# Kernel tuning notes

Measured on AMD Instinct MI355X. Metric: run time of the kernel, lower is better.

The kernel has to match this reference:

```python
import jax, jax.numpy as jnp
import numpy as np

SEQ_LEN = 2048
VOCAB = 32000
N_EMBD = 768
D_INNER = 1536
D_STATE = 16
D_CONV = 4
DT_RANK = 48
N_LAYERS = 2
EPS = 1e-5


def setup_inputs() -> dict:
    key = jax.random.key(0)
    ks = jax.random.split(key, 10)
    s = 0.02
    tokens = jax.random.randint(ks[0], (SEQ_LEN,), 0, VOCAB)
    E = jax.random.normal(ks[1], (VOCAB, N_EMBD)) * s  # tied embedding / lm_head
    in_proj_w = jax.random.normal(ks[2], (N_LAYERS, 2 * D_INNER, N_EMBD)) * s
    conv_w = jax.random.normal(ks[3], (N_LAYERS, D_INNER, 1, D_CONV)) * s  # depthwise
    conv_b = jax.random.normal(ks[4], (N_LAYERS, D_INNER)) * s
    x_proj_w = jax.random.normal(ks[5], (N_LAYERS, DT_RANK + 2 * D_STATE, D_INNER)) * s
    dt_proj_w = jax.random.normal(ks[6], (N_LAYERS, D_INNER, DT_RANK)) * s
    dt_proj_b = jax.random.normal(ks[7], (N_LAYERS, D_INNER)) * s
    # A init exactly as in the module: repeat(arange(1,d_state+1), d_inner).reshape(d_inner, d_state)
    A = jnp.repeat(jnp.arange(1, D_STATE + 1), D_INNER).reshape(D_INNER, D_STATE).astype(jnp.float32)
    A_log = jnp.broadcast_to(jnp.log(A), (N_LAYERS, D_INNER, D_STATE))
    D_param = jnp.ones((N_LAYERS, D_INNER))
    out_proj_w = jax.random.normal(ks[8], (N_LAYERS, N_EMBD, D_INNER)) * s
    norm_w = jnp.ones((N_LAYERS, N_EMBD))
    norm_b = jnp.zeros((N_LAYERS, N_EMBD))
    normf_w = jnp.ones((N_EMBD,))
    normf_b = jnp.zeros((N_EMBD,))
    return {
        'tokens': tokens, 'E': E, 'in_proj_w': in_proj_w, 'conv_w': conv_w,
        'conv_b': conv_b, 'x_proj_w': x_proj_w, 'dt_proj_w': dt_proj_w,
        'dt_proj_b': dt_proj_b, 'A_log': A_log, 'D_param': D_param,
        'out_proj_w': out_proj_w, 'norm_w': norm_w, 'norm_b': norm_b,
        'normf_w': normf_w, 'normf_b': normf_b,
    }


def _rmsnorm(x, w, b):
    inv = jax.lax.rsqrt(jnp.mean(x * x, axis=-1, keepdims=True) + EPS)
    return x * inv * w + b


def _selective_scan(u, delta, A, B, C, D):
    # u,delta: [L, d_inner]; A: [d_inner, d_state]; B,C: [L, d_state]; D: [d_inner]
    dA = jnp.exp(jnp.einsum('ld,dn->ldn', delta, A))            # [L, d_inner, d_state]
    dBu = (delta * u)[:, :, None] * B[:, None, :]               # [L, d_inner, d_state]

    def step(x, inp):
        dA_t, dBu_t, C_t = inp
        x = dA_t * x + dBu_t
        y = x @ C_t                                             # [d_inner]
        return x, y

    x0 = jnp.zeros((D_INNER, D_STATE), dtype=u.dtype)
    _, ys = jax.lax.scan(step, x0, (dA, dBu, C))
    return ys + u * D


def _mamba_block(xn, in_w, cw, cb, xp_w, dt_w, dt_b, a_log, d_p, out_w):
    L = xn.shape[0]
    x_and_res = xn @ in_w.T                                     # [L, 2*d_inner]
    x, res = jnp.split(x_and_res, 2, axis=-1)
    # depthwise causal conv with padding d_conv-1 (both sides), then crop to L
    xc = jax.lax.conv_general_dilated(
        x.T[None], cw, window_strides=(1,), padding=[(D_CONV - 1, D_CONV - 1)],
        feature_group_count=D_INNER, dimension_numbers=('NCH', 'OIH', 'NCH'))[0]
    x = (xc[:, :L] + cb[:, None]).T                             # [L, d_inner]
    x = jax.nn.silu(x)
    # ssm
    A = -jnp.exp(a_log)
    x_dbl = x @ xp_w.T                                          # [L, dt_rank + 2*d_state]
    delta, B, C = jnp.split(x_dbl, [DT_RANK, DT_RANK + D_STATE], axis=-1)
    delta = jax.nn.softplus(delta @ dt_w.T + dt_b)              # [L, d_inner]
    y = _selective_scan(x, delta, A, B, C, d_p)
    y = y * jax.nn.silu(res)
    return y @ out_w.T                                          # [L, n_embd]


def reference(tokens, E, in_proj_w, conv_w, conv_b, x_proj_w, dt_proj_w,
              dt_proj_b, A_log, D_param, out_proj_w, norm_w, norm_b,
              normf_w, normf_b):
    h = E[tokens]                                               # [L, n_embd]
    for i in range(N_LAYERS):
        h = h + _mamba_block(_rmsnorm(h, norm_w[i], norm_b[i]),
                             in_proj_w[i], conv_w[i], conv_b[i], x_proj_w[i],
                             dt_proj_w[i], dt_proj_b[i], A_log[i], D_param[i],
                             out_proj_w[i])
    h = _rmsnorm(h, normf_w, normf_b)
    logits = h @ E.T                                            # tied lm head
    return logits
```

## Files before the change

kernel.cpp:

```cpp
#include <hip/hip_runtime.h>
#include <hip/hip_bf16.h>

#define SEQ   2048
#define NE    768
#define DI    1536
#define DS    16
#define DC    4
#define DTR   48
#define NL    2
#define VOCAB 32000
#define EPS   1e-5f
#define CHUNK 128
#define NCH   (SEQ / CHUNK)

typedef __hip_bfloat16 bf16;
typedef __bf16 bf16x8 __attribute__((ext_vector_type(8)));
typedef float  f32x4  __attribute__((ext_vector_type(4)));

#define GLOBAL_AS __attribute__((address_space(1)))
#define LDS_AS    __attribute__((address_space(3)))

__device__ __forceinline__ void gload16(const void* g, void* l)
{
    __builtin_amdgcn_global_load_lds((const GLOBAL_AS void*)g, (LDS_AS void*)l, 16, 0, 0);
}

__global__ __launch_bounds__(256) void f2b_k(const float* __restrict__ x,
    bf16* __restrict__ y, int n)
{
    int i = (blockIdx.x * 256 + threadIdx.x) * 4;
    if (i >= n) return;
    float4 v = *reinterpret_cast<const float4*>(x + i);
    y[i + 0] = __float2bfloat16(v.x);
    y[i + 1] = __float2bfloat16(v.y);
    y[i + 2] = __float2bfloat16(v.z);
    y[i + 3] = __float2bfloat16(v.w);
}

__global__ __launch_bounds__(256) void embed_k(const int* __restrict__ tok,
    const float* __restrict__ E, float* __restrict__ h)
{
    int l = blockIdx.x;
    int t = tok[l];
    for (int k = threadIdx.x; k < NE; k += 256)
        h[(size_t)l * NE + k] = E[(size_t)t * NE + k];
}

__global__ __launch_bounds__(256) void rmsnorm_k(const float* __restrict__ x,
    const float* __restrict__ w, const float* __restrict__ b, bf16* __restrict__ out)
{
    int l = blockIdx.x;
    const float* xr = x + (size_t)l * NE;
    float ss = 0.f;
    for (int k = threadIdx.x; k < NE; k += 256) { float v = xr[k]; ss += v * v; }
    for (int o = 32; o; o >>= 1) ss += __shfl_down(ss, o);
    __shared__ float s4[4];
    if ((threadIdx.x & 63) == 0) s4[threadIdx.x >> 6] = ss;
    __syncthreads();
    float inv = rsqrtf((s4[0] + s4[1] + s4[2] + s4[3]) / NE + EPS);
    for (int k = threadIdx.x; k < NE; k += 256)
        out[(size_t)l * NE + k] = __float2bfloat16(xr[k] * inv * w[k] + b[k]);
}

__global__ __launch_bounds__(256) void gemm_bt(const bf16* __restrict__ Abf,
    const bf16* __restrict__ Bbf, float* __restrict__ Cout, int M, int N, int K)
{
    __shared__ __align__(16) __bf16 As[128 * 32];
    __shared__ __align__(16) __bf16 Bs[128 * 32];

    const int tid  = threadIdx.x;
    const int wave = tid >> 6;
    const int lane = tid & 63;
    const int wm = wave >> 1, wn = wave & 1;
    const int tm = blockIdx.y * 128;
    const int tn = blockIdx.x * 128;
    const int r16 = lane & 15, quad = lane >> 4;

    const __bf16* A = reinterpret_cast<const __bf16*>(Abf);
    const __bf16* B = reinterpret_cast<const __bf16*>(Bbf);

    const int c0 = tid, c1 = tid + 256;
    const __bf16* ga0 = A + (size_t)(tm + (c0 >> 2)) * K + (c0 & 3) * 8;
    const __bf16* ga1 = A + (size_t)(tm + (c1 >> 2)) * K + (c1 & 3) * 8;
    const __bf16* gb0 = B + (size_t)(tn + (c0 >> 2)) * K + (c0 & 3) * 8;
    const __bf16* gb1 = B + (size_t)(tn + (c1 >> 2)) * K + (c1 & 3) * 8;
    __bf16* la0 = As + c0 * 8;
    __bf16* la1 = As + c1 * 8;
    __bf16* lb0 = Bs + c0 * 8;
    __bf16* lb1 = Bs + c1 * 8;

    f32x4 zero = {0.f, 0.f, 0.f, 0.f};
    f32x4 acc[4][4];
#pragma unroll
    for (int i = 0; i < 4; i++)
#pragma unroll
        for (int j = 0; j < 4; j++) acc[i][j] = zero;

    const int arow = wm * 64 + r16;
    const int brow = wn * 64 + r16;

    for (int kt = 0; kt < K; kt += 32) {
        __syncthreads();
        gload16(ga0 + kt, la0);
        gload16(ga1 + kt, la1);
        gload16(gb0 + kt, lb0);
        gload16(gb1 + kt, lb1);
        __syncthreads();

        bf16x8 av[4], bv[4];
#pragma unroll
        for (int i = 0; i < 4; i++)
            av[i] = *reinterpret_cast<const bf16x8*>(As + (arow + i * 16) * 32 + quad * 8);
#pragma unroll
        for (int j = 0; j < 4; j++)
            bv[j] = *reinterpret_cast<const bf16x8*>(Bs + (brow + j * 16) * 32 + quad * 8);
#pragma unroll
        for (int i = 0; i < 4; i++)
#pragma unroll
            for (int j = 0; j < 4; j++)
                acc[i][j] = __builtin_amdgcn_mfma_f32_16x16x32_bf16(av[i], bv[j], acc[i][j], 0, 0, 0);
    }

#pragma unroll
    for (int i = 0; i < 4; i++) {
        int cm0 = tm + wm * 64 + i * 16 + quad * 4;
#pragma unroll
        for (int j = 0; j < 4; j++) {
            int cn = tn + wn * 64 + j * 16 + r16;
#pragma unroll
            for (int r = 0; r < 4; r++)
                Cout[(size_t)(cm0 + r) * N + cn] = acc[i][j][r];
        }
    }
}

__global__ __launch_bounds__(256) void conv_silu_k(const float* __restrict__ xr,
    const float* __restrict__ cw, const float* __restrict__ cb, float* __restrict__ u)
{
    int idx = blockIdx.x * 256 + threadIdx.x;
    int l = idx / DI, d = idx - l * DI;
    float s = cb[d];
#pragma unroll
    for (int t = 0; t < DC; t++) {
        int ls = l - (DC - 1) + t;
        if (ls >= 0) s += xr[(size_t)ls * (2 * DI) + d] * cw[d * DC + t];
    }
    u[idx] = s / (1.f + expf(-s));
}

__global__ __launch_bounds__(256) void xproj_k(const float* __restrict__ u,
    const float* __restrict__ xpw, float* __restrict__ xdbl)
{
    int gw = blockIdx.x * 4 + (threadIdx.x >> 6);
    int l = gw / 80, j = gw - l * 80;
    int lane = threadIdx.x & 63;
    const float* ur = u + (size_t)l * DI;
    const float* wr = xpw + (size_t)j * DI;
    float s = 0.f;
    for (int k = lane; k < DI; k += 64) s += ur[k] * wr[k];
    for (int o = 32; o; o >>= 1) s += __shfl_down(s, o);
    if (lane == 0) xdbl[(size_t)l * 80 + j] = s;
}

__global__ __launch_bounds__(256) void dtproj_k(const float* __restrict__ xdbl,
    const float* __restrict__ dtw, const float* __restrict__ dtb, float* __restrict__ delta)
{
    int l = blockIdx.y;
    int d = blockIdx.x * 256 + threadIdx.x;
    __shared__ float xs[DTR];
    if (threadIdx.x < DTR) xs[threadIdx.x] = xdbl[(size_t)l * 80 + threadIdx.x];
    __syncthreads();
    float s = dtb[d];
    const float* wr = dtw + (size_t)d * DTR;
#pragma unroll
    for (int k = 0; k < DTR; k++) s += xs[k] * wr[k];
    delta[(size_t)l * DI + d] = fmaxf(s, 0.f) + log1pf(expf(-fabsf(s)));
}

__global__ __launch_bounds__(256) void scan1_k(const float* __restrict__ delta,
    const float* __restrict__ u, const float* __restrict__ xdbl,
    const float* __restrict__ alog, float* __restrict__ S, float* __restrict__ P)
{
    int dg = threadIdx.x >> 4, n = threadIdx.x & 15;
    int d = blockIdx.x * 16 + dg;
    int c = blockIdx.y;
    float A = -expf(alog[(size_t)d * DS + n]);
    float st = 0.f, pr = 1.f;
    int l0 = c * CHUNK;
#pragma unroll 4
    for (int t = 0; t < CHUNK; t++) {
        int l = l0 + t;
        float dl = delta[(size_t)l * DI + d];
        float ul = u[(size_t)l * DI + d];
        float Bn = xdbl[(size_t)l * 80 + DTR + n];
        float a = expf(dl * A);
        st = a * st + dl * ul * Bn;
        pr *= a;
    }
    size_t o = ((size_t)c * DI + d) * DS + n;
    S[o] = st;
    P[o] = pr;
}

__global__ __launch_bounds__(256) void scan2_k(const float* __restrict__ S,
    const float* __restrict__ P, float* __restrict__ sin_)
{
    int i = blockIdx.x * 256 + threadIdx.x;
    float run = 0.f;
#pragma unroll
    for (int c = 0; c < NCH; c++) {
        size_t o = (size_t)c * DI * DS + i;
        sin_[o] = run;
        run = S[o] + P[o] * run;
    }
}

__global__ __launch_bounds__(256) void scan3_k(const float* __restrict__ delta,
    const float* __restrict__ u, const float* __restrict__ xdbl,
    const float* __restrict__ alog, const float* __restrict__ sin_,
    const float* __restrict__ Dp, const float* __restrict__ xr,
    bf16* __restrict__ ybf)
{
    int dg = threadIdx.x >> 4, n = threadIdx.x & 15;
    int d = blockIdx.x * 16 + dg;
    int c = blockIdx.y;
    float A = -expf(alog[(size_t)d * DS + n]);
    float Dv = Dp[d];
    float st = sin_[((size_t)c * DI + d) * DS + n];
    int l0 = c * CHUNK;
#pragma unroll 2
    for (int t = 0; t < CHUNK; t++) {
        int l = l0 + t;
        float dl = delta[(size_t)l * DI + d];
        float ul = u[(size_t)l * DI + d];
        float Bn = xdbl[(size_t)l * 80 + DTR + n];
        float Cn = xdbl[(size_t)l * 80 + DTR + DS + n];
        float a = expf(dl * A);
        st = a * st + dl * ul * Bn;
        float p = st * Cn;
        p += __shfl_down(p, 8);
        p += __shfl_down(p, 4);
        p += __shfl_down(p, 2);
        p += __shfl_down(p, 1);
        if (n == 0) {
            float r = xr[(size_t)l * (2 * DI) + DI + d];
            float yv = (p + ul * Dv) * (r / (1.f + expf(-r)));
            ybf[(size_t)l * DI + d] = __float2bfloat16(yv);
        }
    }
}

__global__ __launch_bounds__(256) void add_k(float* __restrict__ h, const float* __restrict__ t)
{
    int i = blockIdx.x * 256 + threadIdx.x;
    h[i] += t[i];
}

extern "C" void kernel_launch(void* const* d_in, const int* in_sizes, int n_in,
                              void* d_out, int out_size, void* d_ws, size_t ws_size,
                              hipStream_t stream)
{
    const int*   tokens  = (const int*)  d_in[0];
    const float* E       = (const float*)d_in[1];
    const float* in_w    = (const float*)d_in[2];
    const float* conv_w  = (const float*)d_in[3];
    const float* conv_b  = (const float*)d_in[4];
    const float* xp_w    = (const float*)d_in[5];
    const float* dt_w    = (const float*)d_in[6];
    const float* dt_b    = (const float*)d_in[7];
    const float* A_log   = (const float*)d_in[8];
    const float* D_p     = (const float*)d_in[9];
    const float* out_w   = (const float*)d_in[10];
    const float* norm_w  = (const float*)d_in[11];
    const float* norm_b  = (const float*)d_in[12];
    const float* normf_w = (const float*)d_in[13];
    const float* normf_b = (const float*)d_in[14];

    char* ws = (char*)d_ws;
    size_t off = 0;
    auto alloc = [&](size_t bytes) -> void* {
        void* p = ws + off;
        off = (off + bytes + 255) & ~(size_t)255;
        return p;
    };

    float* h     = (float*)alloc((size_t)SEQ * NE * 4);
    bf16*  xn    = (bf16*) alloc((size_t)SEQ * NE * 2);
    float* xr    = (float*)alloc((size_t)SEQ * 2 * DI * 4);
    float* u     = (float*)alloc((size_t)SEQ * DI * 4);
    float* xdbl  = (float*)alloc((size_t)SEQ * 80 * 4);
    float* delta = (float*)alloc((size_t)SEQ * DI * 4);
    bf16*  ybf   = (bf16*) alloc((size_t)SEQ * DI * 2);
    float* tmp   = (float*)alloc((size_t)SEQ * NE * 4);
    bf16*  hf    = (bf16*) alloc((size_t)SEQ * NE * 2);
    bf16*  Ebf   = (bf16*) alloc((size_t)VOCAB * NE * 2);
    bf16*  wbuf  = (bf16*) alloc((size_t)2 * DI * NE * 2);
    float* Sbuf  = (float*)alloc((size_t)NCH * DI * DS * 4);
    float* Pbuf  = (float*)alloc((size_t)NCH * DI * DS * 4);
    float* Sin   = (float*)alloc((size_t)NCH * DI * DS * 4);

    {
        int n = VOCAB * NE;
        f2b_k<<<(n / 4 + 255) / 256, 256, 0, stream>>>(E, Ebf, n);
    }

    embed_k<<<SEQ, 256, 0, stream>>>(tokens, E, h);

    for (int L = 0; L < NL; L++) {
        rmsnorm_k<<<SEQ, 256, 0, stream>>>(h, norm_w + (size_t)L * NE, norm_b + (size_t)L * NE, xn);

        {
            int n = 2 * DI * NE;
            f2b_k<<<(n / 4 + 255) / 256, 256, 0, stream>>>(in_w + (size_t)L * n, wbuf, n);
        }
        gemm_bt<<<dim3(2 * DI / 128, SEQ / 128), 256, 0, stream>>>(
            xn, wbuf, xr, SEQ, 2 * DI, NE);

        conv_silu_k<<<SEQ * DI / 256, 256, 0, stream>>>(
            xr, conv_w + (size_t)L * DI * DC, conv_b + (size_t)L * DI, u);

        xproj_k<<<SEQ * 80 / 4, 256, 0, stream>>>(u, xp_w + (size_t)L * 80 * DI, xdbl);

        dtproj_k<<<dim3(DI / 256, SEQ), 256, 0, stream>>>(
            xdbl, dt_w + (size_t)L * DI * DTR, dt_b + (size_t)L * DI, delta);

        const float* alog = A_log + (size_t)L * DI * DS;
        scan1_k<<<dim3(DI / 16, NCH), 256, 0, stream>>>(delta, u, xdbl, alog, Sbuf, Pbuf);
        scan2_k<<<DI * DS / 256, 256, 0, stream>>>(Sbuf, Pbuf, Sin);
        scan3_k<<<dim3(DI / 16, NCH), 256, 0, stream>>>(
            delta, u, xdbl, alog, Sin, D_p + (size_t)L * DI, xr, ybf);

        {
            int n = NE * DI;
            f2b_k<<<(n / 4 + 255) / 256, 256, 0, stream>>>(out_w + (size_t)L * n, wbuf, n);
        }
        gemm_bt<<<dim3(NE / 128, SEQ / 128), 256, 0, stream>>>(
            ybf, wbuf, tmp, SEQ, NE, DI);

        add_k<<<SEQ * NE / 256, 256, 0, stream>>>(h, tmp);
    }

    rmsnorm_k<<<SEQ, 256, 0, stream>>>(h, normf_w, normf_b, hf);

    gemm_bt<<<dim3(VOCAB / 128, SEQ / 128), 256, 0, stream>>>(
        hf, Ebf, (float*)d_out, SEQ, VOCAB, NE);
}
```

Before: 1.385 ms.

## Swizzle GEMM tiles per XCD, fuse residual add, vectorize xproj, batch dtproj rows

Switches the GEMM to a 1D grid and remaps block IDs so that blocks landing on the same XCD cover contiguous tiles in M-major panel order, aiming for better L2 reuse of B panels (the largest case is the lm_head over the vocabulary). It adds an accumulate flag so the out_proj GEMM adds straight into the residual h, removing the temporary buffer and the separate add kernel. The xproj dot product now uses float4 loads, and dtproj keeps its weight row in registers while looping over 32 sequence positions per block. The register array in dtproj and the extra barriers per row may cost occupancy.

After: 1.194 ms. 13.8% less time.

```diff
diff --git a/kernel.cpp b/kernel.cpp
--- a/kernel.cpp
+++ b/kernel.cpp
@@ -63,17 +63,27 @@
 }
 
 __global__ __launch_bounds__(256) void gemm_bt(const bf16* __restrict__ Abf,
-    const bf16* __restrict__ Bbf, float* __restrict__ Cout, int M, int N, int K)
+    const bf16* __restrict__ Bbf, float* __restrict__ Cout, int M, int N, int K,
+    int accum)
 {
     __shared__ __align__(16) __bf16 As[128 * 32];
     __shared__ __align__(16) __bf16 Bs[128 * 32];
+
+    const int nwg = gridDim.x;
+    const int bid = blockIdx.x;
+    const int q = nwg >> 3, r = nwg & 7;
+    const int xcd = bid & 7, loc = bid >> 3;
+    const int swz = (xcd < r ? xcd * (q + 1) : r * (q + 1) + (xcd - r) * q) + loc;
+    const int mb = M >> 7;
+    const int npan = swz / mb;
+    const int mpan = swz - npan * mb;
+    const int tm = mpan * 128;
+    const int tn = npan * 128;
 
     const int tid  = threadIdx.x;
     const int wave = tid >> 6;
     const int lane = tid & 63;
     const int wm = wave >> 1, wn = wave & 1;
-    const int tm = blockIdx.y * 128;
-    const int tn = blockIdx.x * 128;
     const int r16 = lane & 15, quad = lane >> 4;
 
     const __bf16* A = reinterpret_cast<const __bf16*>(Abf);
@@ -127,9 +137,15 @@
 #pragma unroll
         for (int j = 0; j < 4; j++) {
             int cn = tn + wn * 64 + j * 16 + r16;
-#pragma unroll
-            for (int r = 0; r < 4; r++)
-                Cout[(size_t)(cm0 + r) * N + cn] = acc[i][j][r];
+            if (accum) {
+#pragma unroll
+                for (int rr = 0; rr < 4; rr++)
+                    Cout[(size_t)(cm0 + rr) * N + cn] += acc[i][j][rr];
+            } else {
+#pragma unroll
+                for (int rr = 0; rr < 4; rr++)
+                    Cout[(size_t)(cm0 + rr) * N + cn] = acc[i][j][rr];
+            }
         }
     }
 }
@@ -154,10 +170,14 @@
     int gw = blockIdx.x * 4 + (threadIdx.x >> 6);
     int l = gw / 80, j = gw - l * 80;
     int lane = threadIdx.x & 63;
-    const float* ur = u + (size_t)l * DI;
-    const float* wr = xpw + (size_t)j * DI;
+    const float4* ur = reinterpret_cast<const float4*>(u + (size_t)l * DI);
+    const float4* wr = reinterpret_cast<const float4*>(xpw + (size_t)j * DI);
     float s = 0.f;
-    for (int k = lane; k < DI; k += 64) s += ur[k] * wr[k];
+#pragma unroll
+    for (int k = lane; k < DI / 4; k += 64) {
+        float4 a = ur[k], b = wr[k];
+        s += a.x * b.x + a.y * b.y + a.z * b.z + a.w * b.w;
+    }
     for (int o = 32; o; o >>= 1) s += __shfl_down(s, o);
     if (lane == 0) xdbl[(size_t)l * 80 + j] = s;
 }
@@ -165,16 +185,24 @@
 __global__ __launch_bounds__(256) void dtproj_k(const float* __restrict__ xdbl,
     const float* __restrict__ dtw, const float* __restrict__ dtb, float* __restrict__ delta)
 {
-    int l = blockIdx.y;
     int d = blockIdx.x * 256 + threadIdx.x;
+    float w[DTR];
+    const float* wr = dtw + (size_t)d * DTR;
+#pragma unroll
+    for (int k = 0; k < DTR; k++) w[k] = wr[k];
+    float bv = dtb[d];
     __shared__ float xs[DTR];
-    if (threadIdx.x < DTR) xs[threadIdx.x] = xdbl[(size_t)l * 80 + threadIdx.x];
-    __syncthreads();
-    float s = dtb[d];
-    const float* wr = dtw + (size_t)d * DTR;
-#pragma unroll
-    for (int k = 0; k < DTR; k++) s += xs[k] * wr[k];
-    delta[(size_t)l * DI + d] = fmaxf(s, 0.f) + log1pf(expf(-fabsf(s)));
+    int l0 = blockIdx.y * 32;
+    for (int li = 0; li < 32; li++) {
+        int l = l0 + li;
+        __syncthreads();
+        if (threadIdx.x < DTR) xs[threadIdx.x] = xdbl[(size_t)l * 80 + threadIdx.x];
+        __syncthreads();
+        float s = bv;
+#pragma unroll
+        for (int k = 0; k < DTR; k++) s += xs[k] * w[k];
+        delta[(size_t)l * DI + d] = fmaxf(s, 0.f) + log1pf(expf(-fabsf(s)));
+    }
 }
 
 __global__ __launch_bounds__(256) void scan1_k(const float* __restrict__ delta,
@@ -250,12 +278,6 @@
     }
 }
 
-__global__ __launch_bounds__(256) void add_k(float* __restrict__ h, const float* __restrict__ t)
-{
-    int i = blockIdx.x * 256 + threadIdx.x;
-    h[i] += t[i];
-}
-
 extern "C" void kernel_launch(void* const* d_in, const int* in_sizes, int n_in,
                               void* d_out, int out_size, void* d_ws, size_t ws_size,
                               hipStream_t stream)
@@ -291,7 +313,6 @@
     float* xdbl  = (float*)alloc((size_t)SEQ * 80 * 4);
     float* delta = (float*)alloc((size_t)SEQ * DI * 4);
     bf16*  ybf   = (bf16*) alloc((size_t)SEQ * DI * 2);
-    float* tmp   = (float*)alloc((size_t)SEQ * NE * 4);
     bf16*  hf    = (bf16*) alloc((size_t)SEQ * NE * 2);
     bf16*  Ebf   = (bf16*) alloc((size_t)VOCAB * NE * 2);
     bf16*  wbuf  = (bf16*) alloc((size_t)2 * DI * NE * 2);
@@ -313,15 +334,15 @@
             int n = 2 * DI * NE;
             f2b_k<<<(n / 4 + 255) / 256, 256, 0, stream>>>(in_w + (size_t)L * n, wbuf, n);
         }
-        gemm_bt<<<dim3(2 * DI / 128, SEQ / 128), 256, 0, stream>>>(
-            xn, wbuf, xr, SEQ, 2 * DI, NE);
+        gemm_bt<<<(2 * DI / 128) * (SEQ / 128), 256, 0, stream>>>(
+            xn, wbuf, xr, SEQ, 2 * DI, NE, 0);
 
         conv_silu_k<<<SEQ * DI / 256, 256, 0, stream>>>(
             xr, conv_w + (size_t)L * DI * DC, conv_b + (size_t)L * DI, u);
 
         xproj_k<<<SEQ * 80 / 4, 256, 0, stream>>>(u, xp_w + (size_t)L * 80 * DI, xdbl);
 
-        dtproj_k<<<dim3(DI / 256, SEQ), 256, 0, stream>>>(
+        dtproj_k<<<dim3(DI / 256, SEQ / 32), 256, 0, stream>>>(
             xdbl, dt_w + (size_t)L * DI * DTR, dt_b + (size_t)L * DI, delta);
 
         const float* alog = A_log + (size_t)L * DI * DS;
@@ -334,14 +355,12 @@
             int n = NE * DI;
             f2b_k<<<(n / 4 + 255) / 256, 256, 0, stream>>>(out_w + (size_t)L * n, wbuf, n);
         }
-        gemm_bt<<<dim3(NE / 128, SEQ / 128), 256, 0, stream>>>(
-            ybf, wbuf, tmp, SEQ, NE, DI);
-
-        add_k<<<SEQ * NE / 256, 256, 0, stream>>>(h, tmp);
+        gemm_bt<<<(NE / 128) * (SEQ / 128), 256, 0, stream>>>(
+            ybf, wbuf, h, SEQ, NE, DI, 1);
     }
 
     rmsnorm_k<<<SEQ, 256, 0, stream>>>(h, normf_w, normf_b, hf);
 
-    gemm_bt<<<dim3(VOCAB / 128, SEQ / 128), 256, 0, stream>>>(
-        hf, Ebf, (float*)d_out, SEQ, VOCAB, NE);
-}
+    gemm_bt<<<(VOCAB / 128) * (SEQ / 128), 256, 0, stream>>>(
+        hf, Ebf, (float*)d_out, SEQ, VOCAB, NE, 0);
+}
```
